# Optimization experiments

Hardware: AMD Instinct MI355X
Metric: run time of the kernel (lower is better)

The kernel has to match this reference:

```python
import jax, jax.numpy as jnp
import numpy as np

B, N, C = 4, 1024, 1024
H, TD, MULT = 16, 256, 4
HD = C // H
MAX_LEN = 1024
EPS = 1e-5


def _layer_norm(x, g, b):
    m = jnp.mean(x, axis=-1, keepdims=True)
    v = jnp.mean((x - m) ** 2, axis=-1, keepdims=True)
    return (x - m) / jnp.sqrt(v + EPS) * g + b


def _skew(x):
    # x: [B,H,N,M] -> pad left on last dim, reshape, drop first row -> [B,H,N,M]
    b, h, n, m = x.shape
    x = jnp.pad(x, ((0, 0), (0, 0), (0, 0), (1, 0)))
    x = x.reshape(b, h, m + 1, n)
    return x[:, :, 1:, :]


def setup_inputs() -> dict:
    key = jax.random.key(0)
    ks = jax.random.split(key, 16)
    s = 0.02
    return {
        "x": jax.random.normal(ks[0], (B, N, C), jnp.float32),
        "t": jax.random.normal(ks[1], (B, TD), jnp.float32),
        "ln1_g": jnp.ones((C,), jnp.float32),
        "ln1_b": jnp.zeros((C,), jnp.float32),
        "qkv_w": jax.random.normal(ks[2], (C, 3 * C), jnp.float32) * s,
        "qkv_b": jnp.zeros((3 * C,), jnp.float32),
        "time_w": jax.random.normal(ks[3], (TD, 3 * C), jnp.float32) * s,
        "time_b": jnp.zeros((3 * C,), jnp.float32),
        "out_w": jax.random.normal(ks[4], (C, C), jnp.float32) * s,
        "out_b": jnp.zeros((C,), jnp.float32),
        "Er": jax.random.normal(ks[5], (MAX_LEN, HD), jnp.float32) * s,
        "ln2_g": jnp.ones((C,), jnp.float32),
        "ln2_b": jnp.zeros((C,), jnp.float32),
        "ff1_w": jax.random.normal(ks[6], (C, MULT * C), jnp.float32) * s,
        "ff1_b": jnp.zeros((MULT * C,), jnp.float32),
        "ff2_w": jax.random.normal(ks[7], (MULT * C, C), jnp.float32) * s,
        "ff2_b": jnp.zeros((C,), jnp.float32),
    }


def reference(x, t, ln1_g, ln1_b, qkv_w, qkv_b, time_w, time_b, out_w, out_b,
              Er, ln2_g, ln2_b, ff1_w, ff1_b, ff2_w, ff2_b):
    # ---- attention branch ----
    xn = _layer_norm(x, ln1_g, ln1_b)
    qkv = (xn @ qkv_w + qkv_b).reshape(B, N, 3, H, HD).transpose(2, 0, 3, 1, 4)
    q, k, v = qkv[0], qkv[1], qkv[2]  # [B,H,N,HD]
    tqkv = (t @ time_w + time_b).reshape(B, 1, 3, H, HD).transpose(2, 0, 3, 1, 4)
    q = q + tqkv[0]
    k = k + tqkv[1]
    v = v + tqkv[2]
    Er_n = Er[MAX_LEN - N:]  # [N,HD]
    rel = jnp.einsum('bhnd,md->bhnm', q, Er_n)
    rel = _skew(rel)
    scale = HD ** -0.5
    attn = jnp.einsum('bhnd,bhmd->bhnm', q, k) * scale + rel
    attn = jax.nn.softmax(attn, axis=-1)
    out = jnp.einsum('bhnm,bhmd->bhnd', attn, v)
    out = out.transpose(0, 2, 1, 3).reshape(B, N, C)
    x = x + (out @ out_w + out_b)
    # ---- FFN branch ----
    h = _layer_norm(x, ln2_g, ln2_b)
    h = jax.nn.gelu(h @ ff1_w + ff1_b, approximate=False)
    x = x + (h @ ff2_w + ff2_b)
    return x
```

## Files before the change

### kernel.cpp

```cpp
#include <hip/hip_runtime.h>
#include <hip/hip_bf16.h>

typedef __attribute__((ext_vector_type(8))) short short8;
typedef __attribute__((ext_vector_type(4))) float f32x4;
typedef __attribute__((ext_vector_type(16))) float f32x16;

#define DEV __device__ __forceinline__

DEV float bf2f(ushort u){ union { float f; unsigned int i; } x; x.i = ((unsigned int)u)<<16; return x.f; }
DEV ushort f2bf(float f){ union { float fl; unsigned int i; } x; x.fl = f; unsigned int r = x.i + 0x7fffu + ((x.i>>16)&1u); return (ushort)(r>>16); }

DEV void gl2lds16(const ushort* g, ushort* l){
  __builtin_amdgcn_global_load_lds((const __attribute__((address_space(1))) void*)g,
                                   (__attribute__((address_space(3))) void*)l, 16, 0, 0);
}
DEV f32x16 mfma32(short8 a, short8 b, f32x16 c){
  return __builtin_amdgcn_mfma_f32_32x32x16_bf16(a, b, c, 0, 0, 0);
}
DEV uint cvtpk(float lo, float hi){
  uint r; asm("v_cvt_pk_bf16_f32 %0, %1, %2" : "=v"(r) : "v"(lo), "v"(hi));
  return r;
}
DEV uint q8(float v){
  float c = fminf(fmaxf(v, -127.f), 127.f);
  return ((uint)(int)rintf(c)) & 255u;
}

__global__ void cvt_f2b(const float* __restrict__ in, ushort* __restrict__ out, int n){
  int i = blockIdx.x*blockDim.x + threadIdx.x;
  int stride = gridDim.x*blockDim.x;
  for (; i < n; i += stride) out[i] = f2bf(in[i]);
}

__global__ __launch_bounds__(256) void wt_cvt(const float* __restrict__ in, ushort* __restrict__ out,
                                              int K, int N, int ldk){
  const int n0 = blockIdx.x*64, k0 = blockIdx.y*64;
  __shared__ float T[64][65];
  const int tid = threadIdx.x;
  const int r = tid>>4, c = (tid&15)*4;
  #pragma unroll
  for (int p=0;p<4;p++){
    float4 v = *(const float4*)&in[(size_t)(k0 + p*16 + r)*N + n0 + c];
    T[p*16+r][c+0]=v.x; T[p*16+r][c+1]=v.y; T[p*16+r][c+2]=v.z; T[p*16+r][c+3]=v.w;
  }
  __syncthreads();
  #pragma unroll
  for (int p=0;p<4;p++){
    int n = p*16 + r;
    ushort u0 = f2bf(T[c+0][n]), u1 = f2bf(T[c+1][n]), u2 = f2bf(T[c+2][n]), u3 = f2bf(T[c+3][n]);
    ushort4 u = make_ushort4(u0,u1,u2,u3);
    *(ushort4*)&out[(size_t)(n0+n)*ldk + k0 + c] = u;
  }
}

__global__ __launch_bounds__(256) void vt_k(const ushort* __restrict__ qkv, ushort* __restrict__ vt){
  const int bh = blockIdx.y; const int b = bh>>4, h = bh&15;
  const int n0 = blockIdx.x*64;
  __shared__ ushort T[64][66];
  const int tid = threadIdx.x;
  const int r = tid>>3, c8 = (tid&7)*8;
  #pragma unroll
  for (int p=0;p<2;p++){
    int row = p*32 + r;
    short8 v = *(const short8*)&qkv[(size_t)(b*1024 + n0 + row)*3200 + 2048 + h*64 + c8];
    #pragma unroll
    for (int i=0;i<8;i++) T[row][c8+i] = ((ushort*)&v)[i];
  }
  __syncthreads();
  #pragma unroll
  for (int p=0;p<2;p++){
    int d = p*32 + r;
    union { ushort u[8]; short8 v; } o;
    #pragma unroll
    for (int i=0;i<8;i++) o.u[i] = T[c8+i][d];
    *(short8*)&vt[(size_t)(bh*64 + d)*1152 + n0 + c8] = o.v;
  }
}

__global__ __launch_bounds__(256) void ln_rows(const float* __restrict__ in,
                                               const float* __restrict__ g,
                                               const float* __restrict__ bta,
                                               ushort* __restrict__ out, int ldo){
  int row = blockIdx.x; int tid = threadIdx.x;
  const float* x = in + (size_t)row*1024;
  float v[4]; float s = 0.f;
  #pragma unroll
  for (int i=0;i<4;i++){ v[i] = x[tid + 256*i]; s += v[i]; }
  __shared__ float rbuf[256];
  rbuf[tid] = s; __syncthreads();
  for (int off=128; off>0; off>>=1){ if (tid<off) rbuf[tid]+=rbuf[tid+off]; __syncthreads(); }
  float mean = rbuf[0] * (1.f/1024.f);
  __syncthreads();
  float s2 = 0.f;
  #pragma unroll
  for (int i=0;i<4;i++){ float d=v[i]-mean; s2 += d*d; }
  rbuf[tid] = s2; __syncthreads();
  for (int off=128; off>0; off>>=1){ if (tid<off) rbuf[tid]+=rbuf[tid+off]; __syncthreads(); }
  float var = rbuf[0] * (1.f/1024.f);
  float rstd = rsqrtf(var + 1e-5f);
  #pragma unroll
  for (int i=0;i<4;i++){ int c = tid+256*i; out[(size_t)row*ldo+c] = f2bf((v[i]-mean)*rstd*g[c]+bta[c]); }
}

__global__ __launch_bounds__(256) void tq_gemm2(const float* __restrict__ t, const float* __restrict__ tw,
                                                const float* __restrict__ tb, float* __restrict__ tq){
  const int tid = threadIdx.x;
  const int j = blockIdx.x*64 + (tid & 63);
  const int sl = tid >> 6;
  float acc[4] = {0.f,0.f,0.f,0.f};
  for (int k = sl*64; k < sl*64+64; ++k){
    float wv = tw[(size_t)k*3072 + j];
    #pragma unroll
    for (int b=0;b<4;b++) acc[b] = fmaf(t[b*256+k], wv, acc[b]);
  }
  __shared__ float red[4][4][64];
  #pragma unroll
  for (int b=0;b<4;b++) red[sl][b][tid&63] = acc[b];
  __syncthreads();
  if (sl == 0){
    #pragma unroll
    for (int b=0;b<4;b++)
      tq[b*3072 + j] = red[0][b][tid&63] + red[1][b][tid&63] + red[2][b][tid&63] + red[3][b][tid&63] + tb[j];
  }
}

template<int EPI, int TN>
__global__ __launch_bounds__(256) void gemm4(
    const ushort* __restrict__ A, const ushort* __restrict__ Bt,
    const float* __restrict__ bias, const float* __restrict__ extra,
    ushort* __restrict__ outb, float* __restrict__ outf,
    int K, int lda, int ldb, int ldo, int lde, int nbx)
{
  constexpr int NJ = TN/32;
  __shared__ __align__(16) ushort Al[2][128*32];
  __shared__ __align__(16) ushort Bl[2][TN*32];
  const int nwg = gridDim.x, cpx = nwg >> 3;
  const int bid = blockIdx.x;
  const int swz = (bid & 7)*cpx + (bid >> 3);
  const int m0 = (swz / nbx)*128, n0 = (swz % nbx)*TN;
  const int tid = threadIdx.x, lane = tid & 63, wid = tid >> 6;
  const int wm = (wid&1)*64, wn = (wid>>1)*(TN/2);
  const int l15 = lane&15, l4 = lane>>4;
  f32x4 acc[4][NJ];
  #pragma unroll
  for (int i=0;i<4;i++)
    #pragma unroll
    for (int jx=0;jx<NJ;jx++){ acc[i][jx][0]=0.f; acc[i][jx][1]=0.f; acc[i][jx][2]=0.f; acc[i][jx][3]=0.f; }
  const ushort* a0p = A + (size_t)(m0 + (tid>>2))*lda + (tid&3)*8;
  const ushort* a1p = A + (size_t)(m0 + 64 + (tid>>2))*lda + (tid&3)*8;
  const ushort* b0p = Bt + (size_t)(n0 + (tid>>2))*ldb + (tid&3)*8;
  const ushort* b1p = nullptr;
  if constexpr (TN==128) b1p = Bt + (size_t)(n0 + 64 + (tid>>2))*ldb + (tid&3)*8;
  const int lsl = tid*8, lsh = (tid+256)*8;

  gl2lds16(a0p, &Al[0][lsl]);
  gl2lds16(a1p, &Al[0][lsh]);
  gl2lds16(b0p, &Bl[0][lsl]);
  if constexpr (TN==128) gl2lds16(b1p, &Bl[0][lsh]);
  __syncthreads();

  const int nk = K >> 5;
  for (int it=0; it<nk; ++it){
    const int cur = it & 1;
    ushort* Ac = Al[cur];  ushort* Bc = Bl[cur];
    if (it+1 < nk){
      const int k1 = (it+1) << 5;
      gl2lds16(a0p + k1, &Al[cur^1][lsl]);
      gl2lds16(a1p + k1, &Al[cur^1][lsh]);
      gl2lds16(b0p + k1, &Bl[cur^1][lsl]);
      if constexpr (TN==128) gl2lds16(b1p + k1, &Bl[cur^1][lsh]);
    }
    short8 af[4], bfr[NJ];
    #pragma unroll
    for (int mi=0;mi<4;mi++) af[mi]  = *(const short8*)&Ac[(wm + mi*16 + l15)*32 + l4*8];
    #pragma unroll
    for (int nj=0;nj<NJ;nj++) bfr[nj] = *(const short8*)&Bc[(wn + nj*16 + l15)*32 + l4*8];
    #pragma unroll
    for (int mi=0;mi<4;mi++)
      #pragma unroll
      for (int nj=0;nj<NJ;nj++)
        acc[mi][nj] = __builtin_amdgcn_mfma_f32_16x16x32_bf16(af[mi], bfr[nj], acc[mi][nj], 0,0,0);
    __syncthreads();
  }
  #pragma unroll
  for (int mi=0;mi<4;mi++)
    #pragma unroll
    for (int nj=0;nj<NJ;nj++)
      #pragma unroll
      for (int j=0;j<4;j++){
        int row = m0 + wm + mi*16 + l4*4 + j;
        int col = n0 + wn + nj*16 + l15;
        float v = acc[mi][nj][j] + bias[col];
        if constexpr (EPI==0){ v += extra[(size_t)(row>>10)*lde + col]; outb[(size_t)row*ldo+col] = f2bf(v); }
        else if constexpr (EPI==1){ v += extra[(size_t)row*lde + col]; outf[(size_t)row*ldo+col] = v; }
        else { v = 0.5f*v*(1.f+erff(v*0.70710678118f)); outb[(size_t)row*ldo+col] = f2bf(v); }
      }
}

__global__ __launch_bounds__(256) void relskew8(
    const ushort* __restrict__ qkv, const ushort* __restrict__ Er,
    signed char* __restrict__ srel)
{
  const int bid0 = blockIdx.x;
  const int bid = ((bid0 & 7) << 9) | (bid0 >> 3);
  const int rt = bid & 63, h = (bid>>6)&15, b = bid>>10;
  const int bh = b*16 + h;
  const int r0 = rt*16;
  const int tid = threadIdx.x, w = tid>>6, lane = tid&63;
  const int l15 = lane&15, l4 = lane>>4;
  __shared__ __align__(16) ushort T[17*1032];
  signed char* srb = srel + (size_t)bh*1024*1040;

  if (tid < 17){
    int tgt = r0 - 1 + tid;
    int c = tgt + 1;
    if (tgt >= 0 && c <= 1023) T[tid*1032 + c] = 0;
  }
  const ushort* Qp = qkv + (size_t)b*1024*3200 + h*64;
  short8 qa0 = *(const short8*)(Qp + (size_t)(r0+l15)*3200 + l4*8);
  short8 qa1 = *(const short8*)(Qp + (size_t)(r0+l15)*3200 + 32 + l4*8);
  for (int t=0;t<16;++t){
    const int et = w*16 + t;
    short8 e0 = *(const short8*)(Er + (size_t)(et*16+l15)*64 + l4*8);
    short8 e1 = *(const short8*)(Er + (size_t)(et*16+l15)*64 + 32 + l4*8);
    f32x4 a0 = {0.f,0.f,0.f,0.f};
    a0 = __builtin_amdgcn_mfma_f32_16x16x32_bf16(qa0, e0, a0, 0,0,0);
    a0 = __builtin_amdgcn_mfma_f32_16x16x32_bf16(qa1, e1, a0, 0,0,0);
    const int e = et*16 + l15;
    #pragma unroll
    for (int j=0;j<4;j++){
      int lr = 4*l4 + j;
      int r = r0 + lr;
      ushort v = f2bf(a0[j] * 1.4426950408f);
      bool below = (e >= 1023 - r);
      int ldsrow = below ? (lr + 1) : lr;
      int c = below ? (e + r - 1023) : (e + r + 1);
      T[ldsrow*1032 + c] = v;
    }
  }
  __syncthreads();
  const int c4 = tid*4;
  for (int i=0;i<17;++i){
    int tgt = r0 - 1 + i;
    if (tgt < 0) continue;
    int lo = (i==0) ? (r0+1) : 0;
    int hh = (i==16) ? min(r0+16,1023) : 1023;
    if (c4 >= lo && c4+3 <= hh){
      uint u = q8(bf2f(T[i*1032+c4+0])*64.f)
             | (q8(bf2f(T[i*1032+c4+1])*64.f)<<8)
             | (q8(bf2f(T[i*1032+c4+2])*64.f)<<16)
             | (q8(bf2f(T[i*1032+c4+3])*64.f)<<24);
      *(uint*)(srb + (size_t)tgt*1040 + c4) = u;
    } else if (c4 <= hh && c4+3 >= lo){
      #pragma unroll
      for (int k2=0;k2<4;k2++){
        int c = c4 + k2;
        if (c >= lo && c <= hh)
          srb[(size_t)tgt*1040 + c] = (signed char)(int)q8(bf2f(T[i*1032 + c])*64.f);
      }
    }
  }
}

__global__ __launch_bounds__(256) void attn9(
    const ushort* __restrict__ qkv, const signed char* __restrict__ srel,
    const ushort* __restrict__ Vt, ushort* __restrict__ out)
{
  const int bid0 = blockIdx.x;
  const int swz = (bid0 & 7)*64 + (bid0 >> 3);
  const int bh = swz >> 3, b = bh >> 4, h = bh & 15;
  const int rblk = (swz & 7)*128;
  const int tid = threadIdx.x, w = tid >> 6, lane = tid & 63;
  const int l31 = lane & 31, hi = lane >> 5;
  const int r = rblk + w*32 + l31;
  const ushort* Qp = qkv + (size_t)b*1024*3200 + h*64;
  const ushort* Kp = Qp + 1024;
  const ushort* Vp = Vt + (size_t)bh*64*1152;
  const signed char* Bp = srel + (size_t)bh*1024*1040 + (size_t)r*1040 + hi*4;

  short8 qf0 = *(const short8*)(Qp + (size_t)r*3200 +      hi*8);
  short8 qf1 = *(const short8*)(Qp + (size_t)r*3200 + 16 + hi*8);
  short8 qf2 = *(const short8*)(Qp + (size_t)r*3200 + 32 + hi*8);
  short8 qf3 = *(const short8*)(Qp + (size_t)r*3200 + 48 + hi*8);

  f32x16 O0 = {}, O1 = {};
  float lsum = 0.f;

  short8 kA0 = *(const short8*)(Kp + (size_t)l31*3200 +      hi*8);
  short8 kA1 = *(const short8*)(Kp + (size_t)l31*3200 + 16 + hi*8);
  short8 kA2 = *(const short8*)(Kp + (size_t)l31*3200 + 32 + hi*8);
  short8 kA3 = *(const short8*)(Kp + (size_t)l31*3200 + 48 + hi*8);
  short8 kB0, kB1, kB2, kB3;

  auto step = [&](short8& ka0, short8& ka1, short8& ka2, short8& ka3,
                  short8& kn0, short8& kn1, short8& kn2, short8& kn3, int t){
    const int c0 = t*32;
    if (t < 31){
      const ushort* kp = Kp + (size_t)(c0 + 32 + l31)*3200 + hi*8;
      kn0 = *(const short8*)(kp);
      kn1 = *(const short8*)(kp + 16);
      kn2 = *(const short8*)(kp + 32);
      kn3 = *(const short8*)(kp + 48);
    }
    uint bw[4];
    #pragma unroll
    for (int rq=0;rq<4;rq++) bw[rq] = *(const uint*)(Bp + c0 + rq*8);
    short8 v00 = *(const short8*)(Vp + (size_t)l31*1152      + c0 +      hi*8);
    short8 v01 = *(const short8*)(Vp + (size_t)l31*1152      + c0 + 16 + hi*8);
    short8 v10 = *(const short8*)(Vp + (size_t)(32+l31)*1152 + c0 +      hi*8);
    short8 v11 = *(const short8*)(Vp + (size_t)(32+l31)*1152 + c0 + 16 + hi*8);
    f32x16 S = {};
    __builtin_amdgcn_s_setprio(1);
    S = mfma32(ka0, qf0, S);
    S = mfma32(ka1, qf1, S);
    S = mfma32(ka2, qf2, S);
    S = mfma32(ka3, qf3, S);
    __builtin_amdgcn_s_setprio(0);
    float p[16];
    float s0=0.f, s1=0.f, s2=0.f, s3=0.f;
    #pragma unroll
    for (int rq=0;rq<4;rq++)
      #pragma unroll
      for (int j=0;j<4;j++){
        float bias = (float)(signed char)((bw[rq] >> (8*j)) & 255u) * 0.015625f;
        float pv = __builtin_amdgcn_exp2f(fmaf(S[rq*4+j], 0.18033688f, bias));
        p[rq*4+j] = pv;
        if (j==0) s0 += pv; else if (j==1) s1 += pv; else if (j==2) s2 += pv; else s3 += pv;
      }
    lsum += (s0+s1)+(s2+s3);
    uint W00=cvtpk(p[0],p[1]),   W01=cvtpk(p[2],p[3]);
    uint W10=cvtpk(p[4],p[5]),   W11=cvtpk(p[6],p[7]);
    uint W20=cvtpk(p[8],p[9]),   W21=cvtpk(p[10],p[11]);
    uint W30=cvtpk(p[12],p[13]), W31=cvtpk(p[14],p[15]);
    uint x00 = (uint)__shfl_xor((int)(hi? W00 : W10), 32, 64);
    uint x01 = (uint)__shfl_xor((int)(hi? W01 : W11), 32, 64);
    uint x10 = (uint)__shfl_xor((int)(hi? W20 : W30), 32, 64);
    uint x11 = (uint)__shfl_xor((int)(hi? W21 : W31), 32, 64);
    union { uint u[4]; short8 v; } pf0, pf1;
    pf0.u[0] = hi ? x00 : W00;  pf0.u[1] = hi ? x01 : W01;
    pf0.u[2] = hi ? W10 : x00;  pf0.u[3] = hi ? W11 : x01;
    pf1.u[0] = hi ? x10 : W20;  pf1.u[1] = hi ? x11 : W21;
    pf1.u[2] = hi ? W30 : x10;  pf1.u[3] = hi ? W31 : x11;
    __builtin_amdgcn_s_setprio(1);
    O0 = mfma32(v00, pf0.v, O0);
    O0 = mfma32(v01, pf1.v, O0);
    O1 = mfma32(v10, pf0.v, O1);
    O1 = mfma32(v11, pf1.v, O1);
    __builtin_amdgcn_s_setprio(0);
  };
  for (int t=0;t<32;t+=2){
    step(kA0,kA1,kA2,kA3, kB0,kB1,kB2,kB3, t);
    step(kB0,kB1,kB2,kB3, kA0,kA1,kA2,kA3, t+1);
  }
  float inv = 1.f/(lsum + __shfl_xor(lsum, 32, 64));
  ushort* op = out + ((size_t)(b*1024 + r))*1152 + h*64;
  #pragma unroll
  for (int rq=0;rq<4;rq++)
    #pragma unroll
    for (int s=0;s<2;s++){
      int reg = rq*4 + s*2;
      uint w0 = cvtpk(O0[reg]*inv, O0[reg+1]*inv);
      uint w1 = cvtpk(O1[reg]*inv, O1[reg+1]*inv);
      int d = rq*8 + hi*4 + s*2;
      *(uint*)(op + d) = w0;
      *(uint*)(op + 32 + d) = w1;
    }
}

extern "C" void kernel_launch(void* const* d_in, const int* in_sizes, int n_in,
                              void* d_out, int out_size, void* d_ws, size_t ws_size,
                              hipStream_t stream)
{
  const float* x    = (const float*)d_in[0];
  const float* t    = (const float*)d_in[1];
  const float* ln1g = (const float*)d_in[2];
  const float* ln1b = (const float*)d_in[3];
  const float* qkvw = (const float*)d_in[4];
  const float* qkvb = (const float*)d_in[5];
  const float* timew= (const float*)d_in[6];
  const float* timeb= (const float*)d_in[7];
  const float* outw = (const float*)d_in[8];
  const float* outbv= (const float*)d_in[9];
  const float* Er   = (const float*)d_in[10];
  const float* ln2g = (const float*)d_in[11];
  const float* ln2b = (const float*)d_in[12];
  const float* ff1w = (const float*)d_in[13];
  const float* ff1b = (const float*)d_in[14];
  const float* ff2w = (const float*)d_in[15];
  const float* ff2b = (const float*)d_in[16];
  float* o = (float*)d_out;

  char* ws = (char*)d_ws;
  ushort* qkvw_t = (ushort*)(ws);
  ushort* outw_t = (ushort*)(ws + 7077888);
  ushort* ff1w_t = (ushort*)(ws + 9437184);
  ushort* ff2w_t = (ushort*)(ws + 18874368);
  ushort* er_b   = (ushort*)(ws + 27525120);
  float*  tq     = (float*) (ws + 27656192);
  ushort* bufA   = (ushort*)(ws + 27705344);
  ushort* vt     = (ushort*)(ws + 37142528);
  ushort* bufB   = (ushort*)(ws + 46579712);
  signed char* srel8 = (signed char*)(ws + 81182720);

  wt_cvt<<<dim3(48,16),256,0,stream>>>(qkvw, qkvw_t, 1024, 3072, 1152);
  wt_cvt<<<dim3(16,16),256,0,stream>>>(outw, outw_t, 1024, 1024, 1152);
  wt_cvt<<<dim3(64,16),256,0,stream>>>(ff1w, ff1w_t, 1024, 4096, 1152);
  wt_cvt<<<dim3(16,64),256,0,stream>>>(ff2w, ff2w_t, 4096, 1024, 4224);
  cvt_f2b<<<256,256,0,stream>>>(Er, er_b, 65536);

  ln_rows<<<4096,256,0,stream>>>(x, ln1g, ln1b, bufA, 1152);
  tq_gemm2<<<48,256,0,stream>>>(t, timew, timeb, tq);
  gemm4<0,128><<<768,256,0,stream>>>(bufA, qkvw_t, qkvb, tq, bufB, nullptr,
                                     1024, 1152, 1152, 3200, 3072, 24);
  vt_k<<<dim3(16,64),256,0,stream>>>(bufB, vt);
  relskew8<<<4096,256,0,stream>>>(bufB, er_b, srel8);
  attn9<<<512,256,0,stream>>>(bufB, srel8, vt, bufA);
  gemm4<1,64><<<512,256,0,stream>>>(bufA, outw_t, outbv, x, nullptr, o,
                                    1024, 1152, 1152, 1024, 1024, 16);
  ln_rows<<<4096,256,0,stream>>>(o, ln2g, ln2b, bufA, 1152);
  gemm4<2,128><<<1024,256,0,stream>>>(bufA, ff1w_t, ff1b, nullptr, bufB, nullptr,
                                      1024, 1152, 1152, 4224, 0, 32);
  gemm4<1,64><<<512,256,0,stream>>>(bufB, ff2w_t, ff2b, o, nullptr, o,
                                    4096, 4224, 4224, 1024, 1024, 16);
}
```

Measured before the change: 399.3 us.

## Split attention across KV halves with merge kernel; rework relskew to 32-row int8 tiles

The attention kernel now splits the key/value range into two halves, doubling the grid to 1024 blocks. Each block writes unnormalized fp32 partial outputs and row sums, and a new merge kernel adds the halves and normalizes. This relies on the softmax having no running max, so partials can simply be summed. Separately, the relative-position skew kernel processes 32 rows per block with 32x32 MFMAs and quantizes straight to int8 in LDS with a folded scale, which drops the bf16 round trip and halves the block count. The cost is an extra launch plus fp32 partial-buffer traffic.

```diff
diff --git a/kernel.cpp b/kernel.cpp
--- a/kernel.cpp
+++ b/kernel.cpp
@@ -197,79 +197,88 @@
       }
 }
 
-__global__ __launch_bounds__(256) void relskew8(
+__global__ __launch_bounds__(256) void relskew8_v3(
     const ushort* __restrict__ qkv, const ushort* __restrict__ Er,
     signed char* __restrict__ srel)
 {
   const int bid0 = blockIdx.x;
-  const int bid = ((bid0 & 7) << 9) | (bid0 >> 3);
-  const int rt = bid & 63, h = (bid>>6)&15, b = bid>>10;
-  const int bh = b*16 + h;
-  const int r0 = rt*16;
-  const int tid = threadIdx.x, w = tid>>6, lane = tid&63;
-  const int l15 = lane&15, l4 = lane>>4;
-  __shared__ __align__(16) ushort T[17*1032];
+  const int swz = (bid0 & 7)*256 + (bid0 >> 3);
+  const int bh = swz >> 5, b = bh >> 4, h = bh & 15;
+  const int r0 = (swz & 31)*32;
+  const int tid = threadIdx.x, w = tid >> 6, lane = tid & 63;
+  const int l31 = lane & 31, hi = lane >> 5;
+
+  __shared__ signed char T8[33*1040];
   signed char* srb = srel + (size_t)bh*1024*1040;
 
-  if (tid < 17){
+  if (tid < 33){
     int tgt = r0 - 1 + tid;
     int c = tgt + 1;
-    if (tgt >= 0 && c <= 1023) T[tid*1032 + c] = 0;
-  }
+    if (tgt >= 0 && c <= 1023) T8[tid*1040 + c] = 0;
+  }
+
   const ushort* Qp = qkv + (size_t)b*1024*3200 + h*64;
-  short8 qa0 = *(const short8*)(Qp + (size_t)(r0+l15)*3200 + l4*8);
-  short8 qa1 = *(const short8*)(Qp + (size_t)(r0+l15)*3200 + 32 + l4*8);
-  for (int t=0;t<16;++t){
-    const int et = w*16 + t;
-    short8 e0 = *(const short8*)(Er + (size_t)(et*16+l15)*64 + l4*8);
-    short8 e1 = *(const short8*)(Er + (size_t)(et*16+l15)*64 + 32 + l4*8);
-    f32x4 a0 = {0.f,0.f,0.f,0.f};
-    a0 = __builtin_amdgcn_mfma_f32_16x16x32_bf16(qa0, e0, a0, 0,0,0);
-    a0 = __builtin_amdgcn_mfma_f32_16x16x32_bf16(qa1, e1, a0, 0,0,0);
-    const int e = et*16 + l15;
-    #pragma unroll
-    for (int j=0;j<4;j++){
-      int lr = 4*l4 + j;
-      int r = r0 + lr;
-      ushort v = f2bf(a0[j] * 1.4426950408f);
-      bool below = (e >= 1023 - r);
-      int ldsrow = below ? (lr + 1) : lr;
-      int c = below ? (e + r - 1023) : (e + r + 1);
-      T[ldsrow*1032 + c] = v;
-    }
-  }
-  __syncthreads();
+  const int r = r0 + l31;
+  short8 qf0 = *(const short8*)(Qp + (size_t)r*3200 +      hi*8);
+  short8 qf1 = *(const short8*)(Qp + (size_t)r*3200 + 16 + hi*8);
+  short8 qf2 = *(const short8*)(Qp + (size_t)r*3200 + 32 + hi*8);
+  short8 qf3 = *(const short8*)(Qp + (size_t)r*3200 + 48 + hi*8);
+
+  const float ESC = 92.332481f;
+  for (int t=0; t<8; ++t){
+    const int e0 = w*256 + t*32;
+    const ushort* ep = Er + (size_t)(e0 + l31)*64 + hi*8;
+    short8 ea0 = *(const short8*)(ep);
+    short8 ea1 = *(const short8*)(ep + 16);
+    short8 ea2 = *(const short8*)(ep + 32);
+    short8 ea3 = *(const short8*)(ep + 48);
+    f32x16 acc = {};
+    acc = mfma32(ea0, qf0, acc);
+    acc = mfma32(ea1, qf1, acc);
+    acc = mfma32(ea2, qf2, acc);
+    acc = mfma32(ea3, qf3, acc);
+    #pragma unroll
+    for (int q=0;q<4;q++)
+      #pragma unroll
+      for (int j=0;j<4;j++){
+        int e = e0 + 8*q + 4*hi + j;
+        signed char v = (signed char)(int)q8(acc[4*q+j]*ESC);
+        bool below = (e + r) >= 1023;
+        int i = below ? (l31 + 1) : l31;
+        int c = e + r + (below ? -1023 : 1);
+        T8[i*1040 + c] = v;
+      }
+  }
+  __syncthreads();
+
   const int c4 = tid*4;
-  for (int i=0;i<17;++i){
+  #pragma unroll 4
+  for (int i=0; i<33; ++i){
     int tgt = r0 - 1 + i;
     if (tgt < 0) continue;
     int lo = (i==0) ? (r0+1) : 0;
-    int hh = (i==16) ? min(r0+16,1023) : 1023;
+    int hh = (i==32) ? min(r0+32, 1023) : 1023;
     if (c4 >= lo && c4+3 <= hh){
-      uint u = q8(bf2f(T[i*1032+c4+0])*64.f)
-             | (q8(bf2f(T[i*1032+c4+1])*64.f)<<8)
-             | (q8(bf2f(T[i*1032+c4+2])*64.f)<<16)
-             | (q8(bf2f(T[i*1032+c4+3])*64.f)<<24);
-      *(uint*)(srb + (size_t)tgt*1040 + c4) = u;
+      *(uint*)(srb + (size_t)tgt*1040 + c4) = *(const uint*)&T8[i*1040 + c4];
     } else if (c4 <= hh && c4+3 >= lo){
       #pragma unroll
       for (int k2=0;k2<4;k2++){
         int c = c4 + k2;
-        if (c >= lo && c <= hh)
-          srb[(size_t)tgt*1040 + c] = (signed char)(int)q8(bf2f(T[i*1032 + c])*64.f);
+        if (c >= lo && c <= hh) srb[(size_t)tgt*1040 + c] = T8[i*1040 + c];
       }
     }
   }
 }
 
-__global__ __launch_bounds__(256) void attn9(
+__global__ __launch_bounds__(256) void attn9s(
     const ushort* __restrict__ qkv, const signed char* __restrict__ srel,
-    const ushort* __restrict__ Vt, ushort* __restrict__ out)
+    const ushort* __restrict__ Vt, float* __restrict__ part)
 {
   const int bid0 = blockIdx.x;
-  const int swz = (bid0 & 7)*64 + (bid0 >> 3);
-  const int bh = swz >> 3, b = bh >> 4, h = bh & 15;
-  const int rblk = (swz & 7)*128;
+  const int swz = (bid0 & 7)*128 + (bid0 >> 3);
+  const int bh = swz >> 4, b = bh >> 4, h = bh & 15;
+  const int rblk = ((swz >> 1) & 7)*128;
+  const int kvh = swz & 1;
   const int tid = threadIdx.x, w = tid >> 6, lane = tid & 63;
   const int l31 = lane & 31, hi = lane >> 5;
   const int r = rblk + w*32 + l31;
@@ -286,16 +295,17 @@
   f32x16 O0 = {}, O1 = {};
   float lsum = 0.f;
 
-  short8 kA0 = *(const short8*)(Kp + (size_t)l31*3200 +      hi*8);
-  short8 kA1 = *(const short8*)(Kp + (size_t)l31*3200 + 16 + hi*8);
-  short8 kA2 = *(const short8*)(Kp + (size_t)l31*3200 + 32 + hi*8);
-  short8 kA3 = *(const short8*)(Kp + (size_t)l31*3200 + 48 + hi*8);
+  const int t0 = kvh*16, tend = t0 + 15;
+  short8 kA0 = *(const short8*)(Kp + (size_t)(t0*32 + l31)*3200 +      hi*8);
+  short8 kA1 = *(const short8*)(Kp + (size_t)(t0*32 + l31)*3200 + 16 + hi*8);
+  short8 kA2 = *(const short8*)(Kp + (size_t)(t0*32 + l31)*3200 + 32 + hi*8);
+  short8 kA3 = *(const short8*)(Kp + (size_t)(t0*32 + l31)*3200 + 48 + hi*8);
   short8 kB0, kB1, kB2, kB3;
 
   auto step = [&](short8& ka0, short8& ka1, short8& ka2, short8& ka3,
                   short8& kn0, short8& kn1, short8& kn2, short8& kn3, int t){
     const int c0 = t*32;
-    if (t < 31){
+    if (t < tend){
       const ushort* kp = Kp + (size_t)(c0 + 32 + l31)*3200 + hi*8;
       kn0 = *(const short8*)(kp);
       kn1 = *(const short8*)(kp + 16);
@@ -348,23 +358,41 @@
     O1 = mfma32(v11, pf1.v, O1);
     __builtin_amdgcn_s_setprio(0);
   };
-  for (int t=0;t<32;t+=2){
+  for (int t=t0; t<t0+16; t+=2){
     step(kA0,kA1,kA2,kA3, kB0,kB1,kB2,kB3, t);
     step(kB0,kB1,kB2,kB3, kA0,kA1,kA2,kA3, t+1);
   }
-  float inv = 1.f/(lsum + __shfl_xor(lsum, 32, 64));
-  ushort* op = out + ((size_t)(b*1024 + r))*1152 + h*64;
+  float lrow = lsum + __shfl_xor(lsum, 32, 64);
+
+  float* pp = part + ((size_t)kvh*65536 + (size_t)bh*1024 + r)*68;
   #pragma unroll
   for (int rq=0;rq<4;rq++)
     #pragma unroll
     for (int s=0;s<2;s++){
       int reg = rq*4 + s*2;
-      uint w0 = cvtpk(O0[reg]*inv, O0[reg+1]*inv);
-      uint w1 = cvtpk(O1[reg]*inv, O1[reg+1]*inv);
       int d = rq*8 + hi*4 + s*2;
-      *(uint*)(op + d) = w0;
-      *(uint*)(op + 32 + d) = w1;
+      *(float2*)(pp + d)      = make_float2(O0[reg], O0[reg+1]);
+      *(float2*)(pp + 32 + d) = make_float2(O1[reg], O1[reg+1]);
     }
+  if (hi == 0) pp[64] = lrow;
+}
+
+__global__ __launch_bounds__(256) void attn_merge(const float* __restrict__ part,
+                                                  ushort* __restrict__ out){
+  const int row = blockIdx.x*32 + (threadIdx.x>>3);
+  const int dseg = (threadIdx.x&7)*8;
+  const int bh = row>>10, rr = row&1023, b = bh>>4, h = bh&15;
+  const float* p0 = part + (size_t)row*68;
+  const float* p1 = part + ((size_t)65536 + row)*68;
+  float inv = 1.f/(p0[64] + p1[64]);
+  float4 a0 = *(const float4*)(p0 + dseg), a1 = *(const float4*)(p0 + dseg + 4);
+  float4 b0 = *(const float4*)(p1 + dseg), b1 = *(const float4*)(p1 + dseg + 4);
+  union { uint u[4]; short8 v; } ov;
+  ov.u[0] = cvtpk((a0.x+b0.x)*inv, (a0.y+b0.y)*inv);
+  ov.u[1] = cvtpk((a0.z+b0.z)*inv, (a0.w+b0.w)*inv);
+  ov.u[2] = cvtpk((a1.x+b1.x)*inv, (a1.y+b1.y)*inv);
+  ov.u[3] = cvtpk((a1.z+b1.z)*inv, (a1.w+b1.w)*inv);
+  *(short8*)&out[((size_t)(b*1024 + rr))*1152 + h*64 + dseg] = ov.v;
 }
 
 extern "C" void kernel_launch(void* const* d_in, const int* in_sizes, int n_in,
@@ -401,6 +429,7 @@
   ushort* vt     = (ushort*)(ws + 37142528);
   ushort* bufB   = (ushort*)(ws + 46579712);
   signed char* srel8 = (signed char*)(ws + 81182720);
+  float* part    = (float*)(ws + 150994944);
 
   wt_cvt<<<dim3(48,16),256,0,stream>>>(qkvw, qkvw_t, 1024, 3072, 1152);
   wt_cvt<<<dim3(16,16),256,0,stream>>>(outw, outw_t, 1024, 1024, 1152);
@@ -413,8 +442,9 @@
   gemm4<0,128><<<768,256,0,stream>>>(bufA, qkvw_t, qkvb, tq, bufB, nullptr,
                                      1024, 1152, 1152, 3200, 3072, 24);
   vt_k<<<dim3(16,64),256,0,stream>>>(bufB, vt);
-  relskew8<<<4096,256,0,stream>>>(bufB, er_b, srel8);
-  attn9<<<512,256,0,stream>>>(bufB, srel8, vt, bufA);
+  relskew8_v3<<<2048,256,0,stream>>>(bufB, er_b, srel8);
+  attn9s<<<1024,256,0,stream>>>(bufB, srel8, vt, part);
+  attn_merge<<<2048,256,0,stream>>>(part, bufA);
   gemm4<1,64><<<512,256,0,stream>>>(bufA, outw_t, outbv, x, nullptr, o,
                                     1024, 1152, 1152, 1024, 1024, 16);
   ln_rows<<<4096,256,0,stream>>>(o, ln2g, ln2b, bufA, 1152);
```

New measurement: 391.5 us. No clear change (-1.9%).
